# Performance work log

Measured on AMD Instinct MI355X. Metric: run time of the kernel, lower is better.

Reference implementation:

```python
import jax, jax.numpy as jnp
import numpy as np

B, T, D, H = 4, 2048, 1024, 16
DEPTH = D // H
MASK_NEG = 1e10


def setup_inputs() -> dict:
    key = jax.random.key(0)
    k1, k2, k3 = jax.random.split(key, 3)
    x = jax.random.normal(k1, (B, T, D), dtype=jnp.float32)
    w_attn = jax.random.normal(k2, (D, 3 * D), dtype=jnp.float32) * 0.02
    b_attn = jnp.zeros((3 * D,), dtype=jnp.float32)
    w_proj = jax.random.normal(k3, (D, D), dtype=jnp.float32) * 0.02
    b_proj = jnp.zeros((D,), dtype=jnp.float32)
    return {"x": x, "w_attn": w_attn, "b_attn": b_attn,
            "w_proj": w_proj, "b_proj": b_proj}


def _split_heads(t):
    # (B, T, D) -> (B, H, T, depth)
    return t.reshape(B, T, H, DEPTH).transpose(0, 2, 1, 3)


def reference(x, w_attn, b_attn, w_proj, b_proj):
    # fused QKV projection (GPT-2 conv1d == dense)
    qkv = x @ w_attn + b_attn                      # (B, T, 3D)
    q, k, v = jnp.split(qkv, 3, axis=2)
    q, k, v = _split_heads(q), _split_heads(k), _split_heads(v)
    present = jnp.stack([k, v], axis=1)            # (B, 2, H, T, depth)

    # scaled scores with additive causal mask (as in source: w*b - 1e10*(1-b))
    scores = jnp.einsum('bhqd,bhkd->bhqk', q, k) / jnp.sqrt(
        jnp.asarray(DEPTH, dtype=x.dtype))
    i = jnp.arange(T)[:, None]
    j = jnp.arange(T)[None, :]
    b = (i >= j).astype(scores.dtype)              # (T, T) lower-tri incl diag
    scores = scores * b - MASK_NEG * (1.0 - b)
    attn = jax.nn.softmax(scores, axis=-1)         # (B, H, T, T)

    out = jnp.einsum('bhqk,bhkd->bhqd', attn, v)   # (B, H, T, depth)
    out = out.transpose(0, 2, 1, 3).reshape(B, T, D)
    out = out @ w_proj + b_proj                    # (B, T, D)
    return out, present
```

## Files before the change

### kernel.cpp

```cpp
#include <hip/hip_runtime.h>
#include <hip/hip_bf16.h>
#include <cstdint>
#include <cstddef>

typedef __bf16 y8 __attribute__((ext_vector_type(8)));
typedef float f4 __attribute__((ext_vector_type(4)));
typedef unsigned short u16t;

#define NB 4
#define TT 2048
#define DD 1024
#define HH 16

static constexpr size_t OUT0 = (size_t)NB * TT * DD;
#define QSCALE 0.180336880111120426f

__device__ __forceinline__ u16t bf16r(float f) {
    union { float f; unsigned u; } x; x.f = f;
    return (u16t)((x.u + 0x7FFFu + ((x.u >> 16) & 1u)) >> 16);
}

__device__ __forceinline__ unsigned cvtpk(float lo, float hi) {
    unsigned r;
    asm("v_cvt_pk_bf16_f32 %0, %1, %2" : "=v"(r) : "v"(lo), "v"(hi));
    return r;
}

#define GLDS16(g, s) __builtin_amdgcn_global_load_lds( \
    (__attribute__((address_space(1))) void*)(g),      \
    (__attribute__((address_space(3))) void*)(s), 16, 0, 0)

#define BARX() asm volatile("s_barrier" ::: "memory")
#define VMW(n) asm volatile("s_waitcnt vmcnt(" #n ")" ::: "memory")

__global__ __launch_bounds__(256)
void cvt_f32_bf16(const float* __restrict__ in, u16t* __restrict__ outp, int n) {
    int i = (blockIdx.x * 256 + threadIdx.x) * 8;
    if (i >= n) return;
    float4 a = *(const float4*)(in + i);
    float4 b = *(const float4*)(in + i + 4);
    union { u16t h[8]; uint4 q; } u;
    u.h[0] = bf16r(a.x); u.h[1] = bf16r(a.y); u.h[2] = bf16r(a.z); u.h[3] = bf16r(a.w);
    u.h[4] = bf16r(b.x); u.h[5] = bf16r(b.y); u.h[6] = bf16r(b.z); u.h[7] = bf16r(b.w);
    *(uint4*)(outp + i) = u.q;
}

__global__ __launch_bounds__(256)
void transpose_w(const float* __restrict__ in, u16t* __restrict__ outp, int Kd, int Nd) {
    __shared__ float tile[32][33];
    const int n0 = blockIdx.x * 32, k0 = blockIdx.y * 32;
    const int tx = threadIdx.x & 31, ty = threadIdx.x >> 5;
    for (int yy = ty; yy < 32; yy += 8)
        tile[yy][tx] = in[(size_t)(k0 + yy) * Nd + n0 + tx];
    __syncthreads();
    for (int yy = ty; yy < 32; yy += 8)
        outp[(size_t)(n0 + yy) * Kd + k0 + tx] = bf16r(tile[tx][yy]);
}

template<int MODE, int TPB>
__global__ __launch_bounds__(256, 2)
void gemm_bt(const u16t* __restrict__ A, const u16t* __restrict__ Bt,
             const float* __restrict__ bias, float* __restrict__ C,
             float* __restrict__ pres, u16t* __restrict__ qb,
             u16t* __restrict__ kb, u16t* __restrict__ vtb,
             int N, int K)
{
    __shared__ u16t ldsA[2][128 * 64];
    __shared__ u16t ldsB[2][128 * 64];
    const int tid = threadIdx.x;
    const int w = tid >> 6, l = tid & 63;
    const int wr = w >> 1, wc = w & 1;
    const int lr = l & 15, lq = l >> 4;

    auto stage = [&](int bm, int bn, int k0, int pi) {
#pragma unroll
        for (int c = 0; c < 4; ++c) {
            const int L = ((w * 64 + l) << 4) + (c << 12);
            const int row = L >> 7;
            const int col = (((L >> 4) & 7) ^ (row & 7)) << 3;
            GLDS16(A + (size_t)(bm + row) * K + k0 + col,
                   (char*)ldsA[pi] + (w << 10) + (c << 12));
            GLDS16(Bt + (size_t)(bn + row) * K + k0 + col,
                   (char*)ldsB[pi] + (w << 10) + (c << 12));
        }
    };

    const int nt = K >> 6;

#pragma unroll
    for (int j = 0; j < TPB; ++j) {
        const int idx = blockIdx.x * TPB + j;
        const int bm = (idx & 63) << 7;
        const int bn = (idx >> 6) << 7;

        f4 acc[4][4] = {};
        if (j == 0) stage(bm, bn, 0, 0);

        for (int t = 0; t < nt; ++t) {
            if (t + 1 < nt) {
                stage(bm, bn, (t + 1) << 6, (t + 1) & 1);
            } else if (j + 1 < TPB) {
                const int nx = idx + 1;
                stage((nx & 63) << 7, (nx >> 6) << 7, 0, 0);
            }
            if (t + 1 == nt && j + 1 == TPB) { VMW(0); } else { VMW(8); }
            BARX();
            const char* La = (const char*)ldsA[t & 1];
            const char* Lb = (const char*)ldsB[t & 1];
#pragma unroll
            for (int ks = 0; ks < 2; ++ks) {
                y8 af[4], bfv[4];
#pragma unroll
                for (int m = 0; m < 4; ++m) {
                    const int row = wr * 64 + m * 16 + lr;
                    const int slot = (lq + ks * 4) ^ (row & 7);
                    af[m] = *(const y8*)(La + row * 128 + (slot << 4));
                }
#pragma unroll
                for (int n = 0; n < 4; ++n) {
                    const int row = wc * 64 + n * 16 + lr;
                    const int slot = (lq + ks * 4) ^ (row & 7);
                    bfv[n] = *(const y8*)(Lb + row * 128 + (slot << 4));
                }
#pragma unroll
                for (int m = 0; m < 4; ++m)
#pragma unroll
                    for (int n = 0; n < 4; ++n)
                        acc[m][n] = __builtin_amdgcn_mfma_f32_16x16x32_bf16(af[m], bfv[n], acc[m][n], 0, 0, 0);
            }
            BARX();
        }

        if (MODE == 0) {
#pragma unroll
            for (int m = 0; m < 4; ++m) {
                const int rowb = bm + wr * 64 + m * 16 + 4 * lq;
#pragma unroll
                for (int n = 0; n < 4; ++n) {
                    const int col = bn + wc * 64 + n * 16 + lr;
                    const float bv = bias[col];
#pragma unroll
                    for (int r = 0; r < 4; ++r)
                        C[(size_t)(rowb + r) * N + col] = acc[m][n][r] + bv;
                }
            }
        } else {
            const int part = bn >> 10;
#pragma unroll
            for (int m = 0; m < 4; ++m) {
                const int rowb = bm + wr * 64 + m * 16 + 4 * lq;
                const int b0 = rowb >> 11, t0 = rowb & 2047;
#pragma unroll
                for (int n = 0; n < 4; ++n) {
                    const int colg = bn + wc * 64 + n * 16 + lr;
                    const float bv = bias[colg];
                    const int cl = colg & 1023;
                    const int h = cl >> 6, d = cl & 63;
                    float vals[4];
#pragma unroll
                    for (int r = 0; r < 4; ++r) vals[r] = acc[m][n][r] + bv;
                    if (part == 0) {
#pragma unroll
                        for (int r = 0; r < 4; ++r)
                            qb[(((size_t)(b0 * HH + h)) * TT + t0 + r) * 64 + d] =
                                bf16r(vals[r] * QSCALE);
                    } else if (part == 1) {
#pragma unroll
                        for (int r = 0; r < 4; ++r) {
                            kb[(((size_t)(b0 * HH + h)) * TT + t0 + r) * 64 + d] = bf16r(vals[r]);
                            pres[OUT0 + (((size_t)((b0 * 2 + 0) * HH + h)) * TT + t0 + r) * 64 + d] = vals[r];
                        }
                    } else {
#pragma unroll
                        for (int r = 0; r < 4; ++r)
                            pres[OUT0 + (((size_t)((b0 * 2 + 1) * HH + h)) * TT + t0 + r) * 64 + d] = vals[r];
                        uint2 pk;
                        pk.x = cvtpk(vals[0], vals[1]);
                        pk.y = cvtpk(vals[2], vals[3]);
                        *(uint2*)(vtb + ((size_t)(b0 * HH + h) * 64 + d) * TT + t0) = pk;
                    }
                }
            }
        }
    }
}

__global__ __launch_bounds__(256, 2)
void attn_fwd(const u16t* __restrict__ qg, const u16t* __restrict__ kg,
              const u16t* __restrict__ vtg, u16t* __restrict__ og)
{
    __shared__ u16t sQ[128 * 64];
    __shared__ u16t sK[2 * 64 * 64];
    __shared__ u16t sV[2 * 64 * 64];
    __shared__ u16t sP[4 * 32 * 64];
    const int tid = threadIdx.x;
    const int w = tid >> 6, l = tid & 63;
    const int lr = l & 15, lq = l >> 4;
    const int qt = 15 - blockIdx.y;
    const int bh = blockIdx.x;
    const int b = bh >> 4, h = bh & 15;
    const u16t* qsrc = qg + (size_t)bh * TT * 64;
    const u16t* ksrc = kg + (size_t)bh * TT * 64;
    const u16t* vsrc = vtg + (size_t)bh * 64 * TT;

    auto stageKV = [&](int kt, int pi) {
        const int kv0 = kt << 6;
#pragma unroll
        for (int c = 0; c < 2; ++c) {
            const int L = ((w * 64 + l) << 4) + (c << 12);
            const int row = L >> 7;
            const int col = (((L >> 4) & 7) ^ (row & 7)) << 3;
            GLDS16(ksrc + (kv0 + row) * 64 + col,
                   (char*)sK + (pi << 13) + (w << 10) + (c << 12));
            GLDS16(vsrc + (size_t)row * TT + kv0 + col,
                   (char*)sV + (pi << 13) + (w << 10) + (c << 12));
        }
    };

#pragma unroll
    for (int c = 0; c < 4; ++c) {
        const int L = ((w * 64 + l) << 4) + (c << 12);
        const int row = L >> 7;
        const int col = (((L >> 4) & 7) ^ (row & 7)) << 3;
        GLDS16(qsrc + (qt * 128 + row) * 64 + col, (char*)sQ + (w << 10) + (c << 12));
    }
    stageKV(0, 0);
    __syncthreads();

    y8 qf[2][2];
#pragma unroll
    for (int qm = 0; qm < 2; ++qm)
#pragma unroll
        for (int ks = 0; ks < 2; ++ks) {
            const int row = w * 32 + qm * 16 + lr;
            const int slot = (lq + ks * 4) ^ (row & 7);
            qf[qm][ks] = *(const y8*)((const char*)sQ + row * 128 + (slot << 4));
        }

    f4 o[2][4] = {};
    float mrow[2] = {-1e30f, -1e30f};
    float lsum[2] = {0.f, 0.f};

    char* Pw = (char*)sP + (w << 12);
    const int qmax = qt * 128 + w * 32 + 31;
    const int ktiles = 2 * qt + 2;
    int cur = 0;

    for (int kt = 0; kt < ktiles; ++kt) {
        __syncthreads();
        if (kt + 1 < ktiles) stageKV(kt + 1, cur ^ 1);
        const int kv0 = kt << 6;
        if (kv0 <= qmax) {
            const char* Kb = (const char*)sK + (cur << 13);
            const char* Vb = (const char*)sV + (cur << 13);

            f4 s[2][4] = {};
            __builtin_amdgcn_s_setprio(1);
#pragma unroll
            for (int ks = 0; ks < 2; ++ks) {
                y8 kf[4];
#pragma unroll
                for (int n = 0; n < 4; ++n) {
                    const int row = n * 16 + lr;
                    const int slot = (lq + ks * 4) ^ (row & 7);
                    kf[n] = *(const y8*)(Kb + row * 128 + (slot << 4));
                }
#pragma unroll
                for (int qm = 0; qm < 2; ++qm)
#pragma unroll
                    for (int n = 0; n < 4; ++n)
                        s[qm][n] = __builtin_amdgcn_mfma_f32_16x16x32_bf16(kf[n], qf[qm][ks], s[qm][n], 0, 0, 0);
            }
            __builtin_amdgcn_s_setprio(0);

#pragma unroll
            for (int qm = 0; qm < 2; ++qm) {
                const int qb0 = qt * 128 + w * 32 + qm * 16;
                if (kv0 + 63 > qb0) {
                    const int query = qb0 + lr;
#pragma unroll
                    for (int n = 0; n < 4; ++n)
#pragma unroll
                        for (int r = 0; r < 4; ++r)
                            if (kv0 + n * 16 + 4 * lq + r > query) s[qm][n][r] = -1e30f;
                }

                float mx = -1e30f;
#pragma unroll
                for (int n = 0; n < 4; ++n)
                    mx = fmaxf(mx, fmaxf(fmaxf(s[qm][n][0], s[qm][n][1]),
                                         fmaxf(s[qm][n][2], s[qm][n][3])));
                mx = fmaxf(mx, __shfl_xor(mx, 16));
                mx = fmaxf(mx, __shfl_xor(mx, 32));

                if (!__all(mx <= mrow[qm] + 8.f)) {
                    const float newm = fmaxf(mrow[qm], mx);
                    const float corr = exp2f(mrow[qm] - newm);
                    mrow[qm] = newm;
                    lsum[qm] *= corr;
#pragma unroll
                    for (int n = 0; n < 4; ++n) o[qm][n] *= corr;
                }

                float rs = 0.f;
#pragma unroll
                for (int n = 0; n < 4; ++n)
#pragma unroll
                    for (int r = 0; r < 4; ++r) {
                        const float p = exp2f(s[qm][n][r] - mrow[qm]);
                        s[qm][n][r] = p;
                        rs += p;
                    }
                lsum[qm] += rs;

                const int prow = qm * 16 + lr;
                const int rbase = prow * 128 + ((lq & 1) << 3);
#pragma unroll
                for (int n = 0; n < 4; ++n) {
                    uint2 pk;
                    pk.x = cvtpk(s[qm][n][0], s[qm][n][1]);
                    pk.y = cvtpk(s[qm][n][2], s[qm][n][3]);
                    const int sIdx = 2 * n + (lq >> 1);
                    *(uint2*)(Pw + rbase + ((sIdx ^ (prow & 7)) << 4)) = pk;
                }
            }

            __builtin_amdgcn_s_setprio(1);
#pragma unroll
            for (int ks = 0; ks < 2; ++ks) {
                y8 vf[4], pf[2];
#pragma unroll
                for (int n = 0; n < 4; ++n) {
                    const int row = n * 16 + lr;
                    const int slot = (lq + ks * 4) ^ (row & 7);
                    vf[n] = *(const y8*)(Vb + row * 128 + (slot << 4));
                }
#pragma unroll
                for (int qm = 0; qm < 2; ++qm) {
                    const int row = qm * 16 + lr;
                    const int slot = (lq + ks * 4) ^ (row & 7);
                    pf[qm] = *(const y8*)(Pw + row * 128 + (slot << 4));
                }
#pragma unroll
                for (int qm = 0; qm < 2; ++qm)
#pragma unroll
                    for (int n = 0; n < 4; ++n)
                        o[qm][n] = __builtin_amdgcn_mfma_f32_16x16x32_bf16(vf[n], pf[qm], o[qm][n], 0, 0, 0);
            }
            __builtin_amdgcn_s_setprio(0);
        }
        cur ^= 1;
    }

#pragma unroll
    for (int qm = 0; qm < 2; ++qm) {
        float t = lsum[qm];
        t += __shfl_xor(t, 16);
        t += __shfl_xor(t, 32);
        const float inv = 1.0f / t;
        const int trow = qt * 128 + w * 32 + qm * 16 + lr;
#pragma unroll
        for (int n = 0; n < 4; ++n) {
            uint2 pk;
            pk.x = cvtpk(o[qm][n][0] * inv, o[qm][n][1] * inv);
            pk.y = cvtpk(o[qm][n][2] * inv, o[qm][n][3] * inv);
            *(uint2*)(og + ((size_t)(b * TT + trow)) * DD + h * 64 + n * 16 + 4 * lq) = pk;
        }
    }
}

extern "C" void kernel_launch(void* const* d_in, const int* in_sizes, int n_in,
                              void* d_out, int out_size, void* d_ws, size_t ws_size,
                              hipStream_t stream) {
    const float* x      = (const float*)d_in[0];
    const float* w_attn = (const float*)d_in[1];
    const float* b_attn = (const float*)d_in[2];
    const float* w_proj = (const float*)d_in[3];
    const float* b_proj = (const float*)d_in[4];
    float* outp = (float*)d_out;
    char* ws = (char*)d_ws;

    u16t* xb  = (u16t*)(ws + 0);
    u16t* wta = (u16t*)(ws + 16777216);
    u16t* wtp = (u16t*)(ws + 23068672);
    u16t* qb  = (u16t*)(ws + 25165824);
    u16t* kb  = (u16t*)(ws + 41943040);
    u16t* vtb = (u16t*)(ws + 58720256);
    if (ws_size < 75497472) return;

    cvt_f32_bf16<<<4096, 256, 0, stream>>>(x, xb, 8388608);
    transpose_w<<<dim3(96, 32), 256, 0, stream>>>(w_attn, wta, 1024, 3072);
    transpose_w<<<dim3(32, 32), 256, 0, stream>>>(w_proj, wtp, 1024, 1024);

    gemm_bt<1, 3><<<512, 256, 0, stream>>>(xb, wta, b_attn, nullptr, outp,
                                           qb, kb, vtb, 3072, 1024);
    attn_fwd<<<dim3(64, 16), 256, 0, stream>>>(qb, kb, vtb, xb );
    gemm_bt<0, 1><<<512, 256, 0, stream>>>(xb, wtp, b_proj, outp,
                                           nullptr, nullptr, nullptr, nullptr,
                                           1024, 1024);
}
```

Before: 194.0 us.

## Stage QKV GEMM epilogue through LDS for coalesced vector stores

```diff
diff --git a/kernel.cpp b/kernel.cpp
--- a/kernel.cpp
+++ b/kernel.cpp
@@ -32,6 +32,7 @@
 
 #define BARX() asm volatile("s_barrier" ::: "memory")
 #define VMW(n) asm volatile("s_waitcnt vmcnt(" #n ")" ::: "memory")
+#define LGKM0() asm volatile("s_waitcnt lgkmcnt(0)" ::: "memory")
 
 __global__ __launch_bounds__(256)
 void cvt_f32_bf16(const float* __restrict__ in, u16t* __restrict__ outp, int n) {
@@ -46,15 +47,19 @@
 }
 
 __global__ __launch_bounds__(256)
-void transpose_w(const float* __restrict__ in, u16t* __restrict__ outp, int Kd, int Nd) {
+void transpose_w(const float* __restrict__ in, u16t* __restrict__ outp, int Kd, int Nd,
+                 int qlim, float qs) {
     __shared__ float tile[32][33];
     const int n0 = blockIdx.x * 32, k0 = blockIdx.y * 32;
     const int tx = threadIdx.x & 31, ty = threadIdx.x >> 5;
     for (int yy = ty; yy < 32; yy += 8)
         tile[yy][tx] = in[(size_t)(k0 + yy) * Nd + n0 + tx];
     __syncthreads();
-    for (int yy = ty; yy < 32; yy += 8)
-        outp[(size_t)(n0 + yy) * Kd + k0 + tx] = bf16r(tile[tx][yy]);
+    for (int yy = ty; yy < 32; yy += 8) {
+        float v = tile[tx][yy];
+        if (n0 + yy < qlim) v *= qs;
+        outp[(size_t)(n0 + yy) * Kd + k0 + tx] = bf16r(v);
+    }
 }
 
 template<int MODE, int TPB>
@@ -97,13 +102,8 @@
         if (j == 0) stage(bm, bn, 0, 0);
 
         for (int t = 0; t < nt; ++t) {
-            if (t + 1 < nt) {
-                stage(bm, bn, (t + 1) << 6, (t + 1) & 1);
-            } else if (j + 1 < TPB) {
-                const int nx = idx + 1;
-                stage((nx & 63) << 7, (nx >> 6) << 7, 0, 0);
-            }
-            if (t + 1 == nt && j + 1 == TPB) { VMW(0); } else { VMW(8); }
+            if (t + 1 < nt) { stage(bm, bn, (t + 1) << 6, (t + 1) & 1); VMW(8); }
+            else            { VMW(0); }
             BARX();
             const char* La = (const char*)ldsA[t & 1];
             const char* Lb = (const char*)ldsB[t & 1];
@@ -131,6 +131,11 @@
             BARX();
         }
 
+        if (j + 1 < TPB) {
+            const int nx = idx + 1;
+            stage((nx & 63) << 7, (nx >> 6) << 7, 0, 0);
+        }
+
         if (MODE == 0) {
 #pragma unroll
             for (int m = 0; m < 4; ++m) {
@@ -146,41 +151,81 @@
             }
         } else {
             const int part = bn >> 10;
-#pragma unroll
-            for (int m = 0; m < 4; ++m) {
-                const int rowb = bm + wr * 64 + m * 16 + 4 * lq;
-                const int b0 = rowb >> 11, t0 = rowb & 2047;
-#pragma unroll
-                for (int n = 0; n < 4; ++n) {
-                    const int colg = bn + wc * 64 + n * 16 + lr;
-                    const float bv = bias[colg];
-                    const int cl = colg & 1023;
-                    const int h = cl >> 6, d = cl & 63;
-                    float vals[4];
-#pragma unroll
-                    for (int r = 0; r < 4; ++r) vals[r] = acc[m][n][r] + bv;
-                    if (part == 0) {
-#pragma unroll
-                        for (int r = 0; r < 4; ++r)
-                            qb[(((size_t)(b0 * HH + h)) * TT + t0 + r) * 64 + d] =
-                                bf16r(vals[r] * QSCALE);
-                    } else if (part == 1) {
-#pragma unroll
-                        for (int r = 0; r < 4; ++r) {
-                            kb[(((size_t)(b0 * HH + h)) * TT + t0 + r) * 64 + d] = bf16r(vals[r]);
-                            pres[OUT0 + (((size_t)((b0 * 2 + 0) * HH + h)) * TT + t0 + r) * 64 + d] = vals[r];
-                        }
-                    } else {
-#pragma unroll
-                        for (int r = 0; r < 4; ++r)
-                            pres[OUT0 + (((size_t)((b0 * 2 + 1) * HH + h)) * TT + t0 + r) * 64 + d] = vals[r];
+
+            if (part == 2) {
+#pragma unroll
+                for (int m = 0; m < 4; ++m) {
+                    const int rowb = bm + wr * 64 + m * 16 + 4 * lq;
+                    const int b0 = rowb >> 11, t0 = rowb & 2047;
+#pragma unroll
+                    for (int n = 0; n < 4; ++n) {
+                        const int colg = bn + wc * 64 + n * 16 + lr;
+                        const float bv = bias[colg];
+                        const int cl = colg & 1023;
+                        const int h = cl >> 6, d = cl & 63;
                         uint2 pk;
-                        pk.x = cvtpk(vals[0], vals[1]);
-                        pk.y = cvtpk(vals[2], vals[3]);
+                        pk.x = cvtpk(acc[m][n][0] + bv, acc[m][n][1] + bv);
+                        pk.y = cvtpk(acc[m][n][2] + bv, acc[m][n][3] + bv);
                         *(uint2*)(vtb + ((size_t)(b0 * HH + h) * 64 + d) * TT + t0) = pk;
                     }
                 }
             }
+
+            {
+                char* const half = wr ? (char*)ldsB[1] : (char*)ldsA[1];
+#pragma unroll
+                for (int m = 0; m < 4; ++m)
+#pragma unroll
+                    for (int n = 0; n < 4; ++n) {
+                        const int co = wc * 64 + n * 16 + lr;
+                        float bv = bias[bn + co];
+                        if (part == 0) bv *= QSCALE;
+#pragma unroll
+                        for (int r = 0; r < 4; ++r) {
+                            const int ro = m * 16 + 4 * lq + r;
+                            *(u16t*)(half + ro * 256 + ((((co >> 3) ^ (ro & 7))) << 4)
+                                     + ((co & 7) << 1)) = bf16r(acc[m][n][r] + bv);
+                        }
+                    }
+            }
+            LGKM0();
+            BARX();
+
+            const int hb = (bn & 1023) >> 6;
+#pragma unroll
+            for (int s = 0; s < 8; ++s) {
+                const int sr = s >> 1, sc = s & 1;
+                const int row = sr * 32 + w * 8 + (l >> 3);
+                const char* rh = (row & 64) ? (const char*)ldsB[1] : (const char*)ldsA[1];
+                const int ro = row & 63;
+                const int c = sc * 8 + (l & 7);
+                union { y8 v; uint4 q; u16t h[8]; } u;
+                u.v = *(const y8*)(rh + ro * 256 + ((c ^ (ro & 7)) << 4));
+                const int tglob = bm + row;
+                const int b0 = tglob >> 11, tt = tglob & 2047;
+                const int h2 = hb + sc;
+                const int d0 = (c & 7) * 8;
+                const size_t base = (((size_t)(b0 * HH + h2)) * TT + tt) * 64 + d0;
+                if (part == 0) {
+                    *(uint4*)(qb + base) = u.q;
+                } else {
+                    if (part == 1) *(uint4*)(kb + base) = u.q;
+                    float4 f0, f1;
+                    f0.x = __uint_as_float((unsigned)u.h[0] << 16);
+                    f0.y = __uint_as_float((unsigned)u.h[1] << 16);
+                    f0.z = __uint_as_float((unsigned)u.h[2] << 16);
+                    f0.w = __uint_as_float((unsigned)u.h[3] << 16);
+                    f1.x = __uint_as_float((unsigned)u.h[4] << 16);
+                    f1.y = __uint_as_float((unsigned)u.h[5] << 16);
+                    f1.z = __uint_as_float((unsigned)u.h[6] << 16);
+                    f1.w = __uint_as_float((unsigned)u.h[7] << 16);
+                    const size_t pb = OUT0 +
+                        (((size_t)((b0 * 2 + (part - 1)) * HH + h2)) * TT + tt) * 64 + d0;
+                    *(float4*)(pres + pb) = f0;
+                    *(float4*)(pres + pb + 4) = f1;
+                }
+            }
+            BARX();
         }
     }
 }
@@ -389,8 +434,8 @@
     if (ws_size < 75497472) return;
 
     cvt_f32_bf16<<<4096, 256, 0, stream>>>(x, xb, 8388608);
-    transpose_w<<<dim3(96, 32), 256, 0, stream>>>(w_attn, wta, 1024, 3072);
-    transpose_w<<<dim3(32, 32), 256, 0, stream>>>(w_proj, wtp, 1024, 1024);
+    transpose_w<<<dim3(96, 32), 256, 0, stream>>>(w_attn, wta, 1024, 3072, 1024, QSCALE);
+    transpose_w<<<dim3(32, 32), 256, 0, stream>>>(w_proj, wtp, 1024, 1024, 0, 1.0f);
 
     gemm_bt<1, 3><<<512, 256, 0, stream>>>(xb, wta, b_attn, nullptr, outp,
                                            qb, kb, vtb, 3072, 1024);
```

Result: no change. 197.5 us (+1.8%).
